# Kernel tuning notes

Measured on AMD Instinct MI355X. Metric: run time of the kernel, lower is better.

## Reference

```python
import jax, jax.numpy as jnp
import numpy as np

D_MODEL = 1024
NUM_HEADS = 16
MAX_SEQ_LEN = 2048
THETA = 10000.0
HEAD_DIM = D_MODEL // NUM_HEADS  # 64


def _trunc_normal(key, shape, std):
    # truncated normal in [-3, 3] sigma, matching nn.init.trunc_normal_
    return std * jax.random.truncated_normal(key, -3.0, 3.0, shape, dtype=jnp.float32)


def setup_inputs() -> dict:
    key = jax.random.key(0)
    kx, kq, kk, kv, ko = jax.random.split(key, 5)
    B, L = 2, 2048
    sigma = np.sqrt(2.0 / (D_MODEL + D_MODEL))
    x = jax.random.normal(kx, (B, L, D_MODEL), dtype=jnp.float32)
    token_positions = jnp.arange(L, dtype=jnp.int64 if jax.config.jax_enable_x64 else jnp.int32)[None, :]
    return {
        "x": x,
        "wq": _trunc_normal(kq, (D_MODEL, D_MODEL), sigma),
        "wk": _trunc_normal(kk, (D_MODEL, D_MODEL), sigma),
        "wv": _trunc_normal(kv, (D_MODEL, D_MODEL), sigma),
        "wo": _trunc_normal(ko, (D_MODEL, D_MODEL), sigma),
        "token_positions": token_positions,
    }


def _rope_tables():
    pos = jnp.arange(MAX_SEQ_LEN, dtype=jnp.float32)
    d_idx = jnp.arange(HEAD_DIM // 2, dtype=jnp.float32)
    inv_freq = THETA ** (-2.0 * d_idx / HEAD_DIM)
    angles = pos[:, None] * inv_freq[None, :]  # [max_seq_len, head_dim/2]
    return jnp.cos(angles), jnp.sin(angles)


def _apply_rope(x, cos, sin):
    # x: [b, n, l, h]; cos/sin: [1, l, h/2] (broadcast over b, n)
    xe = x[..., 0::2]
    xo = x[..., 1::2]
    oe = cos * xe - sin * xo
    oo = sin * xe + cos * xo
    # interleave back: stack last axis then flatten pairs
    out = jnp.stack([oe, oo], axis=-1)
    return out.reshape(x.shape)


def reference(x, wq, wk, wv, wo, token_positions):
    B, L, _ = x.shape
    cos_t, sin_t = _rope_tables()
    cos = cos_t[token_positions]  # [1, L, h/2]
    sin = sin_t[token_positions]

    def proj(w):
        y = jnp.einsum('bld,ed->ble', x, w)
        return y.reshape(B, L, NUM_HEADS, HEAD_DIM).transpose(0, 2, 1, 3)  # b n l h

    q, k, v = proj(wq), proj(wk), proj(wv)
    q = _apply_rope(q, cos, sin)
    k = _apply_rope(k, cos, sin)

    scale = 1.0 / np.sqrt(HEAD_DIM).astype(np.float32)
    logits = jnp.einsum('bnqh,bnkh->bnqk', q, k) * scale
    causal = jnp.tril(jnp.ones((L, L), dtype=bool))
    logits = jnp.where(causal[None, None], logits, -jnp.inf)
    scores = jax.nn.softmax(logits, axis=-1)
    out = jnp.einsum('bnqk,bnkh->bnqh', scores, v)
    out = out.transpose(0, 2, 1, 3).reshape(B, L, D_MODEL)
    return jnp.einsum('bld,ed->ble', out, wo)
```

## Files before the change

### kernel.cpp

```cpp
#include <hip/hip_runtime.h>
#include <stdint.h>
#include <stddef.h>

#define SEQ   2048
#define HD    64
#define DM    1024
#define NHEAD 16

typedef __bf16 bf16x8 __attribute__((ext_vector_type(8)));
typedef __bf16 bf16x4 __attribute__((ext_vector_type(4)));
typedef float  f32x4  __attribute__((ext_vector_type(4)));

#define MFMA16x16(a, b, c) __builtin_amdgcn_mfma_f32_16x16x32_bf16((a), (b), (c), 0, 0, 0)

__device__ __forceinline__ void gload16(const void* g, void* lds_uniform) {
    __builtin_amdgcn_global_load_lds(
        (const __attribute__((address_space(1))) uint32_t*)g,
        (__attribute__((address_space(3))) uint32_t*)lds_uniform, 16, 0, 0);
}

__global__ void prep_kernel(const float* __restrict__ x,
                            const float* __restrict__ wq, const float* __restrict__ wk,
                            const float* __restrict__ wv, const float* __restrict__ wo,
                            __bf16* __restrict__ xb, __bf16* __restrict__ wqkv,
                            __bf16* __restrict__ wob,
                            float* __restrict__ ct, float* __restrict__ st) {
    int bid = blockIdx.x;
    if (bid < 4096) {
        int i = (bid * 256 + threadIdx.x) * 4;
        const float4 v = *(const float4*)(x + i);
        __bf16 o[4] = {(__bf16)v.x, (__bf16)v.y, (__bf16)v.z, (__bf16)v.w};
        *(uint64_t*)(xb + i) = *(const uint64_t*)o;
    } else if (bid < 8192) {
        int g = (bid - 4096) >> 10;
        int i = (((bid - 4096) & 1023) * 256 + threadIdx.x) * 4;
        const float* src = (g == 0) ? wq : (g == 1) ? wk : (g == 2) ? wv : wo;
        __bf16* dst = (g == 3) ? wob : (wqkv + (size_t)g * 1048576);
        const float4 v = *(const float4*)(src + i);
        __bf16 o[4] = {(__bf16)v.x, (__bf16)v.y, (__bf16)v.z, (__bf16)v.w};
        *(uint64_t*)(dst + i) = *(const uint64_t*)o;
    } else {
        int i = (bid - 8192) * 256 + threadIdx.x;
        int p = i & 31;
        int pos = i >> 5;
        float freq = expf(-(float)p * (logf(10000.0f) / 32.0f));
        float ang = (float)pos * freq;
        ct[i] = cosf(ang);
        st[i] = sinf(ang);
    }
}

template <int MODE>
__global__ __launch_bounds__(256, 3)
void gemm_bt_kernel(const __bf16* __restrict__ A, const __bf16* __restrict__ W,
                    float* __restrict__ C, __bf16* __restrict__ Qb,
                    __bf16* __restrict__ Kb, __bf16* __restrict__ VTb,
                    const int* __restrict__ tpos, const float* __restrict__ ct,
                    const float* __restrict__ st, int N, int K) {
    __shared__ __align__(16) char smem[32768];
    char* As = smem;
    char* Bs = smem + 16384;
    const int lane = threadIdx.x & 63;
    const int w    = threadIdx.x >> 6;

    const int nbn = N >> 7;
    const int per = (nbn * 32) >> 3;
    const int id  = blockIdx.x;
    const int lin = (id & 7) * per + (id >> 3);
    const int bm  = lin / nbn;
    const int bn  = lin % nbn;

    const int rbase = (w >> 1) * 64;
    const int cbase = (w & 1) * 64;

    f32x4 acc[4][4] = {};

    const int kt_iters = K >> 6;
    for (int kt = 0; kt < kt_iters; ++kt) {
        #pragma unroll
        for (int c = 0; c < 4; ++c) {
            int id2 = (c * 4 + w) * 64 + lane;
            int row = id2 >> 3, cc = id2 & 7;
            int koff = kt * 64 + ((cc ^ (row & 7)) << 3);
            gload16(A + (size_t)(bm * 128 + row) * K + koff, As + (c * 4 + w) * 1024);
            gload16(W + (size_t)(bn * 128 + row) * K + koff, Bs + (c * 4 + w) * 1024);
        }
        __syncthreads();
        #pragma unroll
        for (int ks = 0; ks < 2; ++ks) {
            bf16x8 af[4], bfr[4];
            #pragma unroll
            for (int i = 0; i < 4; ++i) {
                int row = rbase + i * 16 + (lane & 15);
                int c = ks * 4 + (lane >> 4);
                af[i] = *(const bf16x8*)(As + row * 128 + ((c ^ (row & 7)) << 4));
            }
            #pragma unroll
            for (int j = 0; j < 4; ++j) {
                int row = cbase + j * 16 + (lane & 15);
                int c = ks * 4 + (lane >> 4);
                bfr[j] = *(const bf16x8*)(Bs + row * 128 + ((c ^ (row & 7)) << 4));
            }
            #pragma unroll
            for (int i = 0; i < 4; ++i)
                #pragma unroll
                for (int j = 0; j < 4; ++j)
                    acc[i][j] = MFMA16x16(af[i], bfr[j], acc[i][j]);
        }
        __syncthreads();
    }

    if (MODE == 1) {
        #pragma unroll
        for (int i = 0; i < 4; ++i)
            #pragma unroll
            for (int j = 0; j < 4; ++j)
                #pragma unroll
                for (int r = 0; r < 4; ++r) {
                    int m = bm * 128 + rbase + i * 16 + (lane >> 4) * 4 + r;
                    int n = bn * 128 + cbase + j * 16 + (lane & 15);
                    C[(size_t)m * N + n] = acc[i][j][r];
                }
    } else {
        const int which = bn >> 3;
        char* T = smem + w * 8192;
        #pragma unroll
        for (int i = 0; i < 4; ++i)
            #pragma unroll
            for (int j = 0; j < 4; ++j)
                #pragma unroll
                for (int r = 0; r < 4; ++r) {
                    int mi = i * 16 + (lane >> 4) * 4 + r;
                    int ni = j * 16 + (lane & 15);
                    __bf16 v = (__bf16)acc[i][j][r];
                    if (which == 2)
                        *(__bf16*)(T + ni * 128 + ((mi * 2) ^ ((ni & 7) << 4))) = v;
                    else
                        *(__bf16*)(T + mi * 128 + ((ni * 2) ^ ((mi & 7) << 4))) = v;
                }
        #pragma unroll
        for (int it = 0; it < 8; ++it) {
            int id2 = it * 64 + lane;
            int row = id2 >> 3, cc = id2 & 7;
            bf16x8 v = *(const bf16x8*)(T + row * 128 + ((cc ^ (row & 7)) << 4));
            if (which == 2) {
                int n = bn * 128 + cbase + row;
                int m = bm * 128 + rbase + cc * 8;
                int b = m >> 11, l = m & (SEQ - 1);
                int h = (n & (DM - 1)) >> 6, d = n & 63;
                *(bf16x8*)(VTb + ((size_t)((b * NHEAD + h) * HD + d) * SEQ) + l) = v;
            } else {
                int m = bm * 128 + rbase + row;
                int n = bn * 128 + cbase + cc * 8;
                int b = m >> 11, l = m & (SEQ - 1);
                int h = (n & (DM - 1)) >> 6, d = n & 63;
                int pb = tpos[l] * 32 + (d >> 1);
                float sc = (which == 0) ? 0.18033688011112042f : 1.0f;
                bf16x8 ov;
                #pragma unroll
                for (int jj = 0; jj < 4; ++jj) {
                    float cs = ct[pb + jj], sn = st[pb + jj];
                    float e = (float)v[2 * jj], dd = (float)v[2 * jj + 1];
                    ov[2 * jj]     = (__bf16)(sc * (cs * e - sn * dd));
                    ov[2 * jj + 1] = (__bf16)(sc * (sn * e + cs * dd));
                }
                __bf16* dst = which ? Kb : Qb;
                *(bf16x8*)(dst + ((size_t)(b * NHEAD + h) * SEQ + l) * HD + d) = ov;
            }
        }
    }
}

__global__ __launch_bounds__(256, 4)
void attn_kernel(const __bf16* __restrict__ Q, const __bf16* __restrict__ K,
                 const __bf16* __restrict__ VT, __bf16* __restrict__ O) {
    __shared__ __align__(16) char smem[40960];
    const int lane = threadIdx.x & 63;
    const int w    = threadIdx.x >> 6;
    const int tid  = threadIdx.x;
    char* Ps = smem + 32768 + w * 2048;

    const int bid = blockIdx.x;
    const int xcd = bid & 7;
    const int idx = bid >> 3;
    const int bh  = xcd * 4 + (idx & 3);
    const int qb  = 31 - (idx >> 2);

    const __bf16* Qbh  = Q  + (size_t)bh * SEQ * HD;
    const __bf16* Kbh  = K  + (size_t)bh * SEQ * HD;
    const __bf16* VTbh = VT + (size_t)bh * HD * SEQ;
    const int b = bh >> 4, h = bh & 15;

    #pragma unroll
    for (int c = 0; c < 2; ++c) {
        int id = (c * 4 + w) * 64 + lane;
        int row = id >> 3, cc = id & 7;
        int sw = (cc ^ (row & 7)) << 3;
        gload16(Kbh + (size_t)row * HD + sw, smem + (c * 4 + w) * 1024);
        gload16(VTbh + (size_t)row * SEQ + sw, smem + 8192 + (c * 4 + w) * 1024);
    }

    const int qrow = qb * 64 + w * 16 + (lane & 15);
    bf16x8 qf[2];
    qf[0] = *(const bf16x8*)(Qbh + (size_t)qrow * HD + (lane >> 4) * 8);
    qf[1] = *(const bf16x8*)(Qbh + (size_t)qrow * HD + 32 + (lane >> 4) * 8);

    f32x4 o[4] = {};
    float mrow = -1e30f;
    float lrow = 0.f;

    int cur = 0;
    __syncthreads();

    for (int kb = 0; kb <= qb; ++kb) {
        bf16x8 kreg[2], vreg[2];
        if (kb < qb) {
            #pragma unroll
            for (int c = 0; c < 2; ++c) {
                int id = c * 256 + tid;
                int row = id >> 3, cc = id & 7;
                kreg[c] = *(const bf16x8*)(Kbh + (size_t)((kb + 1) * 64 + row) * HD + cc * 8);
                vreg[c] = *(const bf16x8*)(VTbh + (size_t)row * SEQ + (kb + 1) * 64 + cc * 8);
            }
        }

        char* Ks = smem + cur * 16384;
        char* Vs = Ks + 8192;

        f32x4 s[4];
        #pragma unroll
        for (int jt = 0; jt < 4; ++jt) {
            f32x4 z = {};
            #pragma unroll
            for (int ks = 0; ks < 2; ++ks) {
                int row = jt * 16 + (lane & 15);
                int c = ks * 4 + (lane >> 4);
                bf16x8 kf = *(const bf16x8*)(Ks + row * 128 + ((c ^ (row & 7)) << 4));
                z = MFMA16x16(kf, qf[ks], z);
            }
            s[jt] = z;
        }

        if (kb == qb) {
            int i = qb * 64 + w * 16 + (lane & 15);
            #pragma unroll
            for (int jt = 0; jt < 4; ++jt)
                #pragma unroll
                for (int r = 0; r < 4; ++r) {
                    int j = kb * 64 + jt * 16 + (lane >> 4) * 4 + r;
                    if (j > i) s[jt][r] = -1e30f;
                }
        }

        float pmax = fmaxf(fmaxf(fmaxf(s[0][0], s[0][1]), fmaxf(s[0][2], s[0][3])),
                           fmaxf(fmaxf(s[1][0], s[1][1]), fmaxf(s[1][2], s[1][3])));
        pmax = fmaxf(pmax,
               fmaxf(fmaxf(fmaxf(s[2][0], s[2][1]), fmaxf(s[2][2], s[2][3])),
                     fmaxf(fmaxf(s[3][0], s[3][1]), fmaxf(s[3][2], s[3][3]))));

        if (!__all(pmax <= mrow + 8.0f)) {
            pmax = fmaxf(pmax, __shfl_xor(pmax, 16));
            pmax = fmaxf(pmax, __shfl_xor(pmax, 32));
            float mn = fmaxf(mrow, pmax);
            float alpha = exp2f(mrow - mn);
            mrow = mn;
            lrow *= alpha;
            float ar[4];
            #pragma unroll
            for (int r = 0; r < 4; ++r) ar[r] = __shfl(alpha, (lane >> 4) * 4 + r);
            #pragma unroll
            for (int dt = 0; dt < 4; ++dt)
                #pragma unroll
                for (int r = 0; r < 4; ++r)
                    o[dt][r] *= ar[r];
        }

        {
            int qr = lane & 15;
            int swrow = (qr & 7) << 4;
            float rs = 0.f;
            #pragma unroll
            for (int jt = 0; jt < 4; ++jt) {
                bf16x4 pk;
                #pragma unroll
                for (int r = 0; r < 4; ++r) {
                    float pv = exp2f(s[jt][r] - mrow);
                    rs += pv;
                    pk[r] = (__bf16)pv;
                }
                int jj = (jt * 16 + (lane >> 4) * 4) * 2;
                *(bf16x4*)(Ps + qr * 128 + (jj ^ swrow)) = pk;
            }
            lrow += rs;
        }

        #pragma unroll
        for (int js = 0; js < 2; ++js) {
            int prow = lane & 15;
            int cb = js * 4 + (lane >> 4);
            bf16x8 pf = *(const bf16x8*)(Ps + prow * 128 + ((cb ^ (prow & 7)) << 4));
            #pragma unroll
            for (int dt = 0; dt < 4; ++dt) {
                int vrow = dt * 16 + (lane & 15);
                bf16x8 vf = *(const bf16x8*)(Vs + vrow * 128 + ((cb ^ (vrow & 7)) << 4));
                o[dt] = MFMA16x16(pf, vf, o[dt]);
            }
        }

        if (kb < qb) {
            char* Kn = smem + (cur ^ 1) * 16384;
            char* Vn = Kn + 8192;
            #pragma unroll
            for (int c = 0; c < 2; ++c) {
                int id = c * 256 + tid;
                int row = id >> 3, cc = id & 7;
                int sw = (cc ^ (row & 7)) << 4;
                *(bf16x8*)(Kn + row * 128 + sw) = kreg[c];
                *(bf16x8*)(Vn + row * 128 + sw) = vreg[c];
            }
        }
        __syncthreads();
        cur ^= 1;
    }

    lrow += __shfl_xor(lrow, 16);
    lrow += __shfl_xor(lrow, 32);
    float linv[4];
    #pragma unroll
    for (int r = 0; r < 4; ++r) {
        float lr = __shfl(lrow, (lane >> 4) * 4 + r);
        linv[r] = 1.0f / lr;
    }

    char* Os = smem + 32768;
    #pragma unroll
    for (int dt = 0; dt < 4; ++dt)
        #pragma unroll
        for (int r = 0; r < 4; ++r) {
            int orow = w * 16 + (lane >> 4) * 4 + r;
            int oc = (dt * 16 + (lane & 15)) * 2;
            *(__bf16*)(Os + orow * 128 + (oc ^ ((orow & 7) << 4))) = (__bf16)(o[dt][r] * linv[r]);
        }
    __syncthreads();

    #pragma unroll
    for (int c = 0; c < 2; ++c) {
        int id = c * 256 + tid;
        int row = id >> 3, cc = id & 7;
        bf16x8 v = *(const bf16x8*)(Os + row * 128 + ((cc ^ (row & 7)) << 4));
        *(bf16x8*)(O + (size_t)(b * SEQ + qb * 64 + row) * DM + h * HD + cc * 8) = v;
    }
}

extern "C" void kernel_launch(void* const* d_in, const int* in_sizes, int n_in,
                              void* d_out, int out_size, void* d_ws, size_t ws_size,
                              hipStream_t stream) {
    const float* x  = (const float*)d_in[0];
    const float* wq = (const float*)d_in[1];
    const float* wk = (const float*)d_in[2];
    const float* wv = (const float*)d_in[3];
    const float* wo = (const float*)d_in[4];
    const int* tpos = (const int*)d_in[5];
    float* out = (float*)d_out;
    char* ws = (char*)d_ws;

    __bf16* xb   = (__bf16*)(ws);
    __bf16* wqkv = (__bf16*)(ws + (size_t)(8  << 20));
    __bf16* wob  = (__bf16*)(ws + (size_t)(14 << 20));
    __bf16* Qb   = (__bf16*)(ws + (size_t)(16 << 20));
    __bf16* Kb   = (__bf16*)(ws + (size_t)(24 << 20));
    __bf16* VTb  = (__bf16*)(ws + (size_t)(32 << 20));
    __bf16* Ob   = (__bf16*)(ws + (size_t)(40 << 20));
    float* ct    = (float*)(ws + (size_t)(48 << 20));
    float* st    = (float*)(ws + (size_t)(48 << 20) + 262144);

    prep_kernel<<<8448, 256, 0, stream>>>(x, wq, wk, wv, wo, xb, wqkv, wob, ct, st);
    gemm_bt_kernel<0><<<768, 256, 0, stream>>>(xb, wqkv, nullptr, Qb, Kb, VTb,
                                               tpos, ct, st, 3072, 1024);
    attn_kernel<<<1024, 256, 0, stream>>>(Qb, Kb, VTb, Ob);
    gemm_bt_kernel<1><<<256, 256, 0, stream>>>(Ob, wob, out, nullptr, nullptr, nullptr,
                                               nullptr, nullptr, nullptr, 1024, 1024);
}
```

Measured before the change: 108.5 us.

## Compute softmax row sums via MFMA and prioritize MFMA phases in attention loop

The row-sum accumulation moves from scalar adds plus cross-lane shuffles to an extra MFMA that multiplies P by a ones vector, so the sum lands in the same layout as the output accumulator. The PV MFMA block now runs after the next-tile LDS stores, and both MFMA phases are wrapped in s_setprio to favour the matrix-issuing waves. The max reduction is also reordered. The extra MFMA per step adds some matrix work. Using bf16-rounded P for the denominator changes numerics slightly but stays consistent with the numerator.

```diff
diff --git a/kernel.cpp b/kernel.cpp
--- a/kernel.cpp
+++ b/kernel.cpp
@@ -205,9 +205,13 @@
     qf[0] = *(const bf16x8*)(Qbh + (size_t)qrow * HD + (lane >> 4) * 8);
     qf[1] = *(const bf16x8*)(Qbh + (size_t)qrow * HD + 32 + (lane >> 4) * 8);
 
+    bf16x8 ones;
+    #pragma unroll
+    for (int i = 0; i < 8; ++i) ones[i] = (__bf16)1.0f;
+
     f32x4 o[4] = {};
+    f32x4 ls = {};
     float mrow = -1e30f;
-    float lrow = 0.f;
 
     int cur = 0;
     __syncthreads();
@@ -228,6 +232,7 @@
         char* Vs = Ks + 8192;
 
         f32x4 s[4];
+        __builtin_amdgcn_s_setprio(1);
         #pragma unroll
         for (int jt = 0; jt < 4; ++jt) {
             f32x4 z = {};
@@ -240,6 +245,7 @@
             }
             s[jt] = z;
         }
+        __builtin_amdgcn_s_setprio(0);
 
         if (kb == qb) {
             int i = qb * 64 + w * 16 + (lane & 15);
@@ -252,11 +258,11 @@
                 }
         }
 
-        float pmax = fmaxf(fmaxf(fmaxf(s[0][0], s[0][1]), fmaxf(s[0][2], s[0][3])),
-                           fmaxf(fmaxf(s[1][0], s[1][1]), fmaxf(s[1][2], s[1][3])));
-        pmax = fmaxf(pmax,
-               fmaxf(fmaxf(fmaxf(s[2][0], s[2][1]), fmaxf(s[2][2], s[2][3])),
-                     fmaxf(fmaxf(s[3][0], s[3][1]), fmaxf(s[3][2], s[3][3]))));
+        float t0 = fmaxf(fmaxf(fmaxf(s[0][0], s[0][1]), s[0][2]), s[0][3]);
+        float t1 = fmaxf(fmaxf(fmaxf(s[1][0], s[1][1]), s[1][2]), s[1][3]);
+        float t2 = fmaxf(fmaxf(fmaxf(s[2][0], s[2][1]), s[2][2]), s[2][3]);
+        float t3 = fmaxf(fmaxf(fmaxf(s[3][0], s[3][1]), s[3][2]), s[3][3]);
+        float pmax = fmaxf(fmaxf(fmaxf(t0, t1), t2), t3);
 
         if (!__all(pmax <= mrow + 8.0f)) {
             pmax = fmaxf(pmax, __shfl_xor(pmax, 16));
@@ -264,10 +270,11 @@
             float mn = fmaxf(mrow, pmax);
             float alpha = exp2f(mrow - mn);
             mrow = mn;
-            lrow *= alpha;
             float ar[4];
             #pragma unroll
             for (int r = 0; r < 4; ++r) ar[r] = __shfl(alpha, (lane >> 4) * 4 + r);
+            #pragma unroll
+            for (int r = 0; r < 4; ++r) ls[r] *= ar[r];
             #pragma unroll
             for (int dt = 0; dt < 4; ++dt)
                 #pragma unroll
@@ -278,32 +285,14 @@
         {
             int qr = lane & 15;
             int swrow = (qr & 7) << 4;
-            float rs = 0.f;
             #pragma unroll
             for (int jt = 0; jt < 4; ++jt) {
                 bf16x4 pk;
                 #pragma unroll
-                for (int r = 0; r < 4; ++r) {
-                    float pv = exp2f(s[jt][r] - mrow);
-                    rs += pv;
-                    pk[r] = (__bf16)pv;
-                }
+                for (int r = 0; r < 4; ++r)
+                    pk[r] = (__bf16)exp2f(s[jt][r] - mrow);
                 int jj = (jt * 16 + (lane >> 4) * 4) * 2;
                 *(bf16x4*)(Ps + qr * 128 + (jj ^ swrow)) = pk;
-            }
-            lrow += rs;
-        }
-
-        #pragma unroll
-        for (int js = 0; js < 2; ++js) {
-            int prow = lane & 15;
-            int cb = js * 4 + (lane >> 4);
-            bf16x8 pf = *(const bf16x8*)(Ps + prow * 128 + ((cb ^ (prow & 7)) << 4));
-            #pragma unroll
-            for (int dt = 0; dt < 4; ++dt) {
-                int vrow = dt * 16 + (lane & 15);
-                bf16x8 vf = *(const bf16x8*)(Vs + vrow * 128 + ((cb ^ (vrow & 7)) << 4));
-                o[dt] = MFMA16x16(pf, vf, o[dt]);
             }
         }
 
@@ -319,18 +308,30 @@
                 *(bf16x8*)(Vn + row * 128 + sw) = vreg[c];
             }
         }
+
+        __builtin_amdgcn_s_setprio(1);
+        #pragma unroll
+        for (int js = 0; js < 2; ++js) {
+            int prow = lane & 15;
+            int cb = js * 4 + (lane >> 4);
+            bf16x8 pf = *(const bf16x8*)(Ps + prow * 128 + ((cb ^ (prow & 7)) << 4));
+            ls = MFMA16x16(pf, ones, ls);
+            #pragma unroll
+            for (int dt = 0; dt < 4; ++dt) {
+                int vrow = dt * 16 + (lane & 15);
+                bf16x8 vf = *(const bf16x8*)(Vs + vrow * 128 + ((cb ^ (vrow & 7)) << 4));
+                o[dt] = MFMA16x16(pf, vf, o[dt]);
+            }
+        }
+        __builtin_amdgcn_s_setprio(0);
+
         __syncthreads();
         cur ^= 1;
     }
 
-    lrow += __shfl_xor(lrow, 16);
-    lrow += __shfl_xor(lrow, 32);
     float linv[4];
     #pragma unroll
-    for (int r = 0; r < 4; ++r) {
-        float lr = __shfl(lrow, (lane >> 4) * 4 + r);
-        linv[r] = 1.0f / lr;
-    }
+    for (int r = 0; r < 4; ++r) linv[r] = 1.0f / ls[r];
 
     char* Os = smem + 32768;
     #pragma unroll
```

Result: no change. 108.9 us (+0.4%).
